# Optimization experiments

Measured on AMD Instinct MI355X. Metric: run time of the kernel, lower is better.

## Reference

```python
import jax, jax.numpy as jnp
import numpy as np

WIN = 11          # win_size
NC = 2            # num_classes
SMOOTH = 0.1      # smoothing / (num_classes - 1) = 0.1/1; fix_flag=True and 0.1 <= Max_Smootning=0.2


def setup_inputs() -> dict:
    key = jax.random.key(0)
    k1, k2 = jax.random.split(key)
    x = jax.random.normal(k1, (8, 2, 1024, 1024), dtype=jnp.float32)
    target = jax.random.randint(k2, (8, 1, 1024, 1024), 0, 2, dtype=jnp.int32)
    return {"x": x, "target": target}


def reference(x, target):
    kern = -jnp.ones((1, 1, WIN, WIN), dtype=jnp.float32)
    kern = kern.at[0, 0, WIN // 2, WIN // 2].set(float(WIN * WIN - 1))

    tf = target.astype(jnp.float32)  # [B,1,H,W]
    pad = WIN // 2
    edge = jax.lax.conv_general_dilated(tf, kern, window_strides=(1, 1),
                                        padding=[(pad, pad), (pad, pad)])
    edge = jnp.where(edge != 0, 1.0, 0.0)  # [B,1,H,W], 1 near label edges

    log_p = jax.nn.log_softmax(x, axis=1)  # [B,C,H,W]

    # One-hot masks (to_categorical with alpha=0 and alpha=smoothing).
    oh = jax.nn.one_hot(target[:, 0], NC, dtype=jnp.float32)  # [B,H,W,C]
    oh = jnp.transpose(oh, (0, 3, 1, 2))                      # [B,C,H,W]
    # alpha everywhere, 1 - alpha + alpha/NC at the true class
    soft = SMOOTH + oh * (1.0 - 2.0 * SMOOTH + SMOOTH / NC)

    mask = oh * (1.0 - edge) + soft * edge  # hard label off-edge, smoothed on-edge
    loss = jnp.mean(jnp.sum(mask * log_p, axis=1))
    return -loss
```

## Files before the change

### kernel.cpp

```cpp
#include <hip/hip_runtime.h>

#define HH 1024
#define WW 1024
#define BB 8
#define TILE 64
#define HALO 5
#define TROWS 74
#define TB    76
#define TD    19
#define HP    65

__global__ __launch_bounds__(256) void ls_main(const float* __restrict__ x,
                                               const int* __restrict__ tgt,
                                               double* __restrict__ acc_out) {
    __shared__ int s_t[TROWS * TD];
    __shared__ int s_h[TROWS * HP];
    __shared__ float s_red[4];
    unsigned char* s_tb = (unsigned char*)s_t;

    const int tid = threadIdx.x;
    const int b  = blockIdx.z;
    const int ty = blockIdx.y * TILE;
    const int tx = blockIdx.x * TILE;
    const int ty0 = ty - HALO;
    const int tx0 = tx - HALO;

    const int* tb_g = tgt + (size_t)b * HH * WW;

    for (int d = tid; d < TROWS * TD; d += 256) {
        int r = d / TD;
        int dc = d - r * TD;
        int gy = ty0 + r;
        int c0 = dc * 4;
        unsigned int pk = 0;
        if ((unsigned)gy < HH) {
#pragma unroll
            for (int bnum = 0; bnum < 4; ++bnum) {
                int c = c0 + bnum;
                int gx = tx0 + c;
                if (c < TROWS && (unsigned)gx < WW)
                    pk |= ((unsigned int)tb_g[gy * WW + gx]) << (8 * bnum);
            }
        }
        s_t[d] = (int)pk;
    }
    __syncthreads();

    if (tid < 222) {
        int row = tid / 3;
        int seg = tid - row * 3;
        int cbeg = seg * 22;
        int cend = (seg == 2) ? 64 : cbeg + 22;
        int base = row * TB + cbeg;
        int W = 0;
#pragma unroll
        for (int k = 0; k < 11; ++k) W += s_tb[base + k];
        int hb = row * HP;
        for (int c = cbeg; c < cend; ++c) {
            s_h[hb + c] = W;
            W += (int)s_tb[row * TB + c + 11] - (int)s_tb[row * TB + c];
        }
    }
    __syncthreads();

    const float* x0p = x + ((size_t)b * 2 + 0) * HH * WW;
    const float* x1p = x + ((size_t)b * 2 + 1) * HH * WW;

    const int col   = tid & 63;
    const int chunk = tid >> 6;
    const int r0    = chunk * 16;

    int V = 0;
#pragma unroll
    for (int k = 0; k < 11; ++k) V += s_h[(r0 + k) * HP + col];

    float acc = 0.f;
#pragma unroll
    for (int j = 0; j < 16; ++j) {
        int row = r0 + j;
        int t = s_tb[(row + HALO) * TB + (col + HALO)];
        bool edge = (121 * t != V);
        if (j != 15)
            V += s_h[(row + 11) * HP + col] - s_h[row * HP + col];

        size_t gidx = (size_t)(ty + row) * WW + (tx + col);
        float xv0 = x0p[gidx];
        float xv1 = x1p[gidx];
        float m   = fmaxf(xv0, xv1);
        float lse = m + __logf(1.0f + __expf(-fabsf(xv0 - xv1)));
        float lp0 = xv0 - lse, lp1 = xv1 - lse;
        float lpt = t ? lp1 : lp0;
        float lpo = t ? lp0 : lp1;
        acc += edge ? (0.95f * lpt + 0.1f * lpo) : lpt;
    }

#pragma unroll
    for (int off = 32; off > 0; off >>= 1) acc += __shfl_down(acc, off, 64);
    if ((tid & 63) == 0) s_red[tid >> 6] = acc;
    __syncthreads();
    if (tid == 0) {
        float bs = s_red[0] + s_red[1] + s_red[2] + s_red[3];
        atomicAdd(acc_out, (double)bs);
    }
}

__global__ void ls_final(const double* __restrict__ acc, float* __restrict__ out) {
    out[0] = (float)(-acc[0] * (1.0 / (8.0 * 1024.0 * 1024.0)));
}

extern "C" void kernel_launch(void* const* d_in, const int* in_sizes, int n_in,
                              void* d_out, int out_size, void* d_ws, size_t ws_size,
                              hipStream_t stream) {
    const float* x  = (const float*)d_in[0];
    const int* tgt  = (const int*)d_in[1];
    double* acc     = (double*)d_ws;

    hipMemsetAsync(d_ws, 0, sizeof(double), stream);
    dim3 grid(WW / TILE, HH / TILE, BB);
    hipLaunchKernelGGL(ls_main, grid, dim3(256), 0, stream, x, tgt, acc);
    hipLaunchKernelGGL(ls_final, dim3(1), dim3(1), 0, stream, acc, (float*)d_out);
}
```

Baseline: 142.1 us.

## Prefetch x as float4 per-thread rows, vectorize target loads, drop atomics

Each thread now handles 16 contiguous pixels of one row, loading both logit channels as float4 vectors at kernel start so the global loads overlap the target staging and box-sum work. Target halo loads use int4 vector reads with a padded shared tile, and the separable box filter switches to vertical sums first and then a horizontal slide per thread. The global double atomic plus memset is replaced by per-block partials reduced by a 256-thread final kernel. The cost is higher register pressure from the 32 prefetched floats, and the per-thread row layout may cause shared memory bank conflicts on the s_v accesses.

```diff
diff --git a/kernel.cpp b/kernel.cpp
--- a/kernel.cpp
+++ b/kernel.cpp
@@ -6,15 +6,15 @@
 #define TILE 64
 #define HALO 5
 #define TROWS 74
-#define TB    76
-#define TD    19
-#define HP    65
+#define TB    80
+#define VP    65
+#define NBLK  (16*16*8)
 
 __global__ __launch_bounds__(256) void ls_main(const float* __restrict__ x,
                                                const int* __restrict__ tgt,
-                                               double* __restrict__ acc_out) {
-    __shared__ int s_t[TROWS * TD];
-    __shared__ int s_h[TROWS * HP];
+                                               float* __restrict__ partial) {
+    __shared__ int   s_t[TROWS * (TB / 4)];
+    __shared__ int   s_v[74 * VP];
     __shared__ float s_red[4];
     unsigned char* s_tb = (unsigned char*)s_t;
 
@@ -23,72 +23,79 @@
     const int ty = blockIdx.y * TILE;
     const int tx = blockIdx.x * TILE;
     const int ty0 = ty - HALO;
-    const int tx0 = tx - HALO;
+
+    const int row = tid >> 2;
+    const int c0  = (tid & 3) << 4;
+    const float* x0p = x + ((size_t)b * 2 + 0) * HH * WW + (size_t)(ty + row) * WW + tx + c0;
+    const float* x1p = x + ((size_t)b * 2 + 1) * HH * WW + (size_t)(ty + row) * WW + tx + c0;
+    float4 xv0[4], xv1[4];
+#pragma unroll
+    for (int q = 0; q < 4; ++q) xv0[q] = ((const float4*)x0p)[q];
+#pragma unroll
+    for (int q = 0; q < 4; ++q) xv1[q] = ((const float4*)x1p)[q];
+    const float* f0 = (const float*)xv0;
+    const float* f1 = (const float*)xv1;
 
     const int* tb_g = tgt + (size_t)b * HH * WW;
 
-    for (int d = tid; d < TROWS * TD; d += 256) {
-        int r = d / TD;
-        int dc = d - r * TD;
-        int gy = ty0 + r;
-        int c0 = dc * 4;
+    for (int i = tid; i < TROWS * (TB / 4); i += 256) {
+        int r  = i / (TB / 4);
+        int ch = i - r * (TB / 4);
+        int gy  = ty0 + r;
+        int gx0 = tx - 8 + ch * 4;
         unsigned int pk = 0;
         if ((unsigned)gy < HH) {
+            if (gx0 >= 0 && gx0 + 3 < WW) {
+                int4 v = *(const int4*)(tb_g + (size_t)gy * WW + gx0);
+                pk = (unsigned)v.x | ((unsigned)v.y << 8) |
+                     ((unsigned)v.z << 16) | ((unsigned)v.w << 24);
+            } else {
 #pragma unroll
-            for (int bnum = 0; bnum < 4; ++bnum) {
-                int c = c0 + bnum;
-                int gx = tx0 + c;
-                if (c < TROWS && (unsigned)gx < WW)
-                    pk |= ((unsigned int)tb_g[gy * WW + gx]) << (8 * bnum);
+                for (int k = 0; k < 4; ++k) {
+                    int gx = gx0 + k;
+                    if ((unsigned)gx < WW)
+                        pk |= ((unsigned)tb_g[(size_t)gy * WW + gx]) << (8 * k);
+                }
             }
         }
-        s_t[d] = (int)pk;
+        s_t[i] = (int)pk;
     }
     __syncthreads();
 
-    if (tid < 222) {
-        int row = tid / 3;
-        int seg = tid - row * 3;
-        int cbeg = seg * 22;
-        int cend = (seg == 2) ? 64 : cbeg + 22;
-        int base = row * TB + cbeg;
-        int W = 0;
+    for (int i = tid; i < 296; i += 256) {
+        int cc = 3 + (i >> 2);
+        int r0 = (i & 3) << 4;
+        int V = 0;
 #pragma unroll
-        for (int k = 0; k < 11; ++k) W += s_tb[base + k];
-        int hb = row * HP;
-        for (int c = cbeg; c < cend; ++c) {
-            s_h[hb + c] = W;
-            W += (int)s_tb[row * TB + c + 11] - (int)s_tb[row * TB + c];
+        for (int k = 0; k < 11; ++k) V += s_tb[(r0 + k) * TB + cc];
+        int base = (cc - 3) * VP;
+        for (int r = r0; r < r0 + 16; ++r) {
+            s_v[base + r] = V;
+            if (r != r0 + 15) V += (int)s_tb[(r + 11) * TB + cc] - (int)s_tb[r * TB + cc];
         }
     }
     __syncthreads();
 
-    const float* x0p = x + ((size_t)b * 2 + 0) * HH * WW;
-    const float* x1p = x + ((size_t)b * 2 + 1) * HH * WW;
+    int W = 0;
+#pragma unroll
+    for (int d = 0; d < 11; ++d) W += s_v[(c0 + d) * VP + row];
 
-    const int col   = tid & 63;
-    const int chunk = tid >> 6;
-    const int r0    = chunk * 16;
-
-    int V = 0;
-#pragma unroll
-    for (int k = 0; k < 11; ++k) V += s_h[(r0 + k) * HP + col];
+    const unsigned long long* tp =
+        (const unsigned long long*)(s_tb + (row + HALO) * TB + c0 + 8);
+    unsigned long long tlo = tp[0], thi = tp[1];
 
     float acc = 0.f;
 #pragma unroll
-    for (int j = 0; j < 16; ++j) {
-        int row = r0 + j;
-        int t = s_tb[(row + HALO) * TB + (col + HALO)];
-        bool edge = (121 * t != V);
-        if (j != 15)
-            V += s_h[(row + 11) * HP + col] - s_h[row * HP + col];
+    for (int jj = 0; jj < 16; ++jj) {
+        int t = (int)((jj < 8 ? (tlo >> (8 * jj)) : (thi >> (8 * (jj - 8)))) & 1);
+        bool edge = (121 * t != W);
+        if (jj != 15)
+            W += s_v[(c0 + jj + 11) * VP + row] - s_v[(c0 + jj) * VP + row];
 
-        size_t gidx = (size_t)(ty + row) * WW + (tx + col);
-        float xv0 = x0p[gidx];
-        float xv1 = x1p[gidx];
-        float m   = fmaxf(xv0, xv1);
-        float lse = m + __logf(1.0f + __expf(-fabsf(xv0 - xv1)));
-        float lp0 = xv0 - lse, lp1 = xv1 - lse;
+        float a0 = f0[jj], a1 = f1[jj];
+        float m   = fmaxf(a0, a1);
+        float lse = m + __logf(1.0f + __expf(-fabsf(a0 - a1)));
+        float lp0 = a0 - lse, lp1 = a1 - lse;
         float lpt = t ? lp1 : lp0;
         float lpo = t ? lp0 : lp1;
         acc += edge ? (0.95f * lpt + 0.1f * lpo) : lpt;
@@ -99,13 +106,25 @@
     if ((tid & 63) == 0) s_red[tid >> 6] = acc;
     __syncthreads();
     if (tid == 0) {
-        float bs = s_red[0] + s_red[1] + s_red[2] + s_red[3];
-        atomicAdd(acc_out, (double)bs);
+        int bid = (blockIdx.z * gridDim.y + blockIdx.y) * gridDim.x + blockIdx.x;
+        partial[bid] = s_red[0] + s_red[1] + s_red[2] + s_red[3];
     }
 }
 
-__global__ void ls_final(const double* __restrict__ acc, float* __restrict__ out) {
-    out[0] = (float)(-acc[0] * (1.0 / (8.0 * 1024.0 * 1024.0)));
+__global__ __launch_bounds__(256) void ls_final(const float* __restrict__ partial,
+                                                float* __restrict__ out) {
+    __shared__ double s_red[4];
+    const int tid = threadIdx.x;
+    double s = 0.0;
+    for (int i = tid; i < NBLK; i += 256) s += (double)partial[i];
+#pragma unroll
+    for (int off = 32; off > 0; off >>= 1) s += __shfl_down(s, off, 64);
+    if ((tid & 63) == 0) s_red[tid >> 6] = s;
+    __syncthreads();
+    if (tid == 0) {
+        double total = s_red[0] + s_red[1] + s_red[2] + s_red[3];
+        out[0] = (float)(-total * (1.0 / (8.0 * 1024.0 * 1024.0)));
+    }
 }
 
 extern "C" void kernel_launch(void* const* d_in, const int* in_sizes, int n_in,
@@ -113,10 +132,9 @@
                               hipStream_t stream) {
     const float* x  = (const float*)d_in[0];
     const int* tgt  = (const int*)d_in[1];
-    double* acc     = (double*)d_ws;
+    float* partial  = (float*)d_ws;
 
-    hipMemsetAsync(d_ws, 0, sizeof(double), stream);
     dim3 grid(WW / TILE, HH / TILE, BB);
-    hipLaunchKernelGGL(ls_main, grid, dim3(256), 0, stream, x, tgt, acc);
-    hipLaunchKernelGGL(ls_final, dim3(1), dim3(1), 0, stream, acc, (float*)d_out);
+    hipLaunchKernelGGL(ls_main, grid, dim3(256), 0, stream, x, tgt, partial);
+    hipLaunchKernelGGL(ls_final, dim3(1), dim3(256), 0, stream, partial, (float*)d_out);
 }
```

Measured after the change: 126.0 us. 11.3% less time.
